# Performance work log

Hardware: AMD Instinct MI355X
Metric: run time of the kernel (lower is better)

The kernel has to match this reference:

```python
import jax, jax.numpy as jnp
import numpy as np

N, E, D, ED, G = 50000, 800000, 64, 32, 50


def setup_inputs() -> dict:
    key = jax.random.key(0)
    ks = jax.random.split(key, 24)
    s = 0.05
    inp = {
        "x": jax.random.normal(ks[0], (N, D), jnp.float32),
        "edge_attr": jax.random.normal(ks[1], (E, ED), jnp.float32),
        "edge_index": jax.random.randint(ks[2], (2, E), 0, N, jnp.int64),
    }
    i = 3
    for step in range(2):
        inp[f"fe{step}_W1"] = jax.random.normal(ks[i], (2 * D + ED, D), jnp.float32) * s; i += 1
        inp[f"fe{step}_b1"] = jnp.zeros((D,), jnp.float32)
        inp[f"fe{step}_W2"] = jax.random.normal(ks[i], (D, D), jnp.float32) * s; i += 1
        inp[f"fe{step}_b2"] = jnp.zeros((D,), jnp.float32)
        inp[f"lstm{step}_Wih"] = jax.random.normal(ks[i], (D, 4 * D), jnp.float32) * s; i += 1
        inp[f"lstm{step}_Whh"] = jax.random.normal(ks[i], (D, 4 * D), jnp.float32) * s; i += 1
        inp[f"lstm{step}_bih"] = jnp.zeros((4 * D,), jnp.float32)
        inp[f"lstm{step}_bhh"] = jnp.zeros((4 * D,), jnp.float32)
    inp["gm_W"] = jax.random.normal(ks[i], (D, G), jnp.float32) * s; i += 1
    inp["gm_b"] = jnp.zeros((G,), jnp.float32)
    inp["fm_W"] = jax.random.normal(ks[i], (D, G), jnp.float32) * s; i += 1
    inp["fm_b"] = jnp.zeros((G,), jnp.float32)
    return inp


def _mpn(x, edge_attr, src, dst, W1, b1, W2, b2):
    # x_i = x[dst] (target), x_j = x[src] (source); aggregate 'add' at dst
    m = jnp.concatenate([x[dst], x[src], edge_attr], axis=1)  # [E, 2D+ED]
    m = jax.nn.relu(m @ W1 + b1) @ W2 + b2                    # [E, D]
    return jax.ops.segment_sum(m, dst, num_segments=x.shape[0])


def _lstm_cell(inp, h, c, Wih, Whh, bih, bhh):
    gates = inp @ Wih + h @ Whh + (bih + bhh)  # [N, 4D], gate order i,f,g,o
    i, f, g, o = jnp.split(gates, 4, axis=1)
    c = jax.nn.sigmoid(f) * c + jax.nn.sigmoid(i) * jnp.tanh(g)
    h = jax.nn.sigmoid(o) * jnp.tanh(c)
    return h, c


def reference(x, edge_attr, edge_index,
              fe0_W1, fe0_b1, fe0_W2, fe0_b2,
              lstm0_Wih, lstm0_Whh, lstm0_bih, lstm0_bhh,
              fe1_W1, fe1_b1, fe1_W2, fe1_b2,
              lstm1_Wih, lstm1_Whh, lstm1_bih, lstm1_bhh,
              gm_W, gm_b, fm_W, fm_b):
    src, dst = edge_index[0], edge_index[1]
    c = jnp.zeros_like(x)
    fes = [(fe0_W1, fe0_b1, fe0_W2, fe0_b2), (fe1_W1, fe1_b1, fe1_W2, fe1_b2)]
    lstms = [(lstm0_Wih, lstm0_Whh, lstm0_bih, lstm0_bhh),
             (lstm1_Wih, lstm1_Whh, lstm1_bih, lstm1_bhh)]
    for step in range(2):
        a = _mpn(x, edge_attr, src, dst, *fes[step])
        # LSTMCell(input=x, (h=a, c=c)) as in the original forward
        x, c = _lstm_cell(x, a, c, *lstms[step])
    g = jax.nn.sigmoid(x @ gm_W + gm_b)   # [N, G]
    h_v_G = x @ fm_W + fm_b               # [N, G]
    return jnp.sum(g * h_v_G, axis=0)     # [G]
```

## Files before the change

kernel.cpp:

```cpp
#include <hip/hip_runtime.h>
#include <hip/hip_bf16.h>

using short8 = __attribute__((ext_vector_type(8))) short;
using f32x4  = __attribute__((ext_vector_type(4))) float;

#define KLP 136

__device__ __forceinline__ unsigned short f2bf(float f) {
  unsigned u = __float_as_uint(f);
  u += 0x7FFFu + ((u >> 16) & 1u);
  return (unsigned short)(u >> 16);
}
__device__ __forceinline__ unsigned pack2(float a, float b) {
  return (unsigned)f2bf(a) | ((unsigned)f2bf(b) << 16);
}
#if __has_builtin(__builtin_amdgcn_rcpf)
__device__ __forceinline__ float fast_rcp(float x) { return __builtin_amdgcn_rcpf(x); }
#else
__device__ __forceinline__ float fast_rcp(float x) { return 1.f / x; }
#endif
__device__ __forceinline__ float sigm(float x) { return fast_rcp(1.f + __expf(-x)); }
__device__ __forceinline__ float tanh_f(float x) { return fmaf(2.f, sigm(2.f * x), -1.f); }

__global__ __launch_bounds__(256) void prep_simple(
    const float* __restrict__ W1_0, const float* __restrict__ Wih0,
    const float* __restrict__ bih0, const float* __restrict__ bhh0,
    const float* __restrict__ W1_1, const float* __restrict__ Wih1,
    const float* __restrict__ bih1, const float* __restrict__ bhh1,
    const float* __restrict__ gmW, const float* __restrict__ fmW,
    unsigned short* __restrict__ W1T,
    unsigned short* __restrict__ WcT,
    float* __restrict__ bG,
    unsigned short* __restrict__ WrT)
{
  int t = blockIdx.x * 256 + threadIdx.x;
  const int per = 10240 + 16384 + 256;
  if (t >= 2 * per + 8192) return;
  if (t >= 2 * per) {
    int r2 = t - 2 * per;
    int o = r2 >> 6, k = r2 & 63;
    float v = 0.f;
    if (o < 50) v = gmW[k * 50 + o];
    else if (o >= 64 && o < 114) v = fmW[k * 50 + (o - 64)];
    WrT[o * 64 + k] = f2bf(v);
    return;
  }
  int step = t / per, r = t % per;
  const float* W1  = step ? W1_1 : W1_0;
  const float* Wih = step ? Wih1 : Wih0;
  const float* bih = step ? bih1 : bih0;
  const float* bhh = step ? bhh1 : bhh0;
  if (r < 10240) {
    int o = r / 160, k = r % 160;
    W1T[step * 10240 + o * 160 + k] = f2bf(W1[k * 64 + o]);
  } else if (r < 26624) {
    int rr = r - 10240;
    int g = rr >> 6, k = rr & 63;
    WcT[step * 32768 + g * 128 + k] = f2bf(Wih[k * 256 + g]);
  } else {
    int g = r - 26624;
    bG[step * 256 + g] = bih[g] + bhh[g];
  }
}

__global__ __launch_bounds__(256) void prep_merge(
    const float* __restrict__ W2_0, const float* __restrict__ Whh0, const float* __restrict__ b2_0,
    const float* __restrict__ W2_1, const float* __restrict__ Whh1, const float* __restrict__ b2_1,
    unsigned short* __restrict__ WcT,
    float* __restrict__ b2h)
{
  int t = blockIdx.x * 256 + threadIdx.x;
  if (t < 32768) {
    int step = t >> 14, r = t & 16383;
    int g = r >> 6, k = r & 63;
    const float* W2  = step ? W2_1 : W2_0;
    const float* Whh = step ? Whh1 : Whh0;
    float v = 0.f;
    for (int j = 0; j < 64; ++j) v = fmaf(W2[k * 64 + j], Whh[j * 256 + g], v);
    WcT[step * 32768 + g * 128 + 64 + k] = f2bf(v);
  } else if (t < 33280) {
    int r = t - 32768;
    int step = r >> 8, g = r & 255;
    const float* b2  = step ? b2_1 : b2_0;
    const float* Whh = step ? Whh1 : Whh0;
    float v = 0.f;
    for (int j = 0; j < 64; ++j) v = fmaf(b2[j], Whh[j * 256 + g], v);
    b2h[step * 256 + g] = v;
  }
}

__global__ __launch_bounds__(256) void convert_x(
    const float* __restrict__ x, unsigned short* __restrict__ xb, int n)
{
  int i = blockIdx.x * 256 + threadIdx.x;
  if (i < n) xb[i] = f2bf(x[i]);
}

__global__ __launch_bounds__(256) void hist_kernel(
    const int* __restrict__ dstI, int* __restrict__ hist, int E)
{
  int e = blockIdx.x * 256 + threadIdx.x;
  if (e < E) atomicAdd(&hist[dstI[e]], 1);
}

__global__ __launch_bounds__(256) void scan_part(
    const int* __restrict__ hist, int2* __restrict__ blockTot, int N)
{
  __shared__ int sD[256], sS[256];
  int t = threadIdx.x;
  int n = blockIdx.x * 256 + t;
  int d = (n < N) ? hist[n] : 0;
  int sg = (d + 15) >> 4;
  sD[t] = d; sS[t] = sg;
  __syncthreads();
  #pragma unroll
  for (int off = 128; off; off >>= 1) {
    if (t < off) { sD[t] += sD[t + off]; sS[t] += sS[t + off]; }
    __syncthreads();
  }
  if (t == 0) blockTot[blockIdx.x] = make_int2(sD[0], sS[0]);
}

__global__ __launch_bounds__(256) void scan_mid(
    const int2* __restrict__ blockTot, int2* __restrict__ blockBase,
    int* __restrict__ nSegTot, int nb)
{
  __shared__ int sD[256], sS[256];
  int t = threadIdx.x;
  int d = 0, s = 0;
  if (t < nb) { int2 v = blockTot[t]; d = v.x; s = v.y; }
  sD[t] = d; sS[t] = s;
  __syncthreads();
  #pragma unroll
  for (int off = 1; off < 256; off <<= 1) {
    int vd = (t >= off) ? sD[t - off] : 0;
    int vs = (t >= off) ? sS[t - off] : 0;
    __syncthreads();
    sD[t] += vd; sS[t] += vs;
    __syncthreads();
  }
  if (t < nb) blockBase[t] = make_int2(sD[t] - d, sS[t] - s);
  if (t == nb - 1) *nSegTot = sS[t];
}

__global__ __launch_bounds__(256) void scan_final(
    const int* __restrict__ hist, const int2* __restrict__ blockBase,
    int* __restrict__ cursor, int4* __restrict__ segInfo, int N)
{
  __shared__ int sD[256], sS[256];
  int t = threadIdx.x;
  int n = blockIdx.x * 256 + t;
  int d = (n < N) ? hist[n] : 0;
  int sg = (d + 15) >> 4;
  sD[t] = d; sS[t] = sg;
  __syncthreads();
  #pragma unroll
  for (int off = 1; off < 256; off <<= 1) {
    int vd = (t >= off) ? sD[t - off] : 0;
    int vs = (t >= off) ? sS[t - off] : 0;
    __syncthreads();
    sD[t] += vd; sS[t] += vs;
    __syncthreads();
  }
  if (n < N) {
    int2 bb = blockBase[blockIdx.x];
    int degBase = bb.x + sD[t] - d;
    int segBase = bb.y + sS[t] - sg;
    cursor[n] = degBase;
    for (int j = 0; j < sg; ++j)
      segInfo[segBase + j] = make_int4(degBase + j * 16, n, min(d - j * 16, 16), 0);
  }
}

__global__ __launch_bounds__(256) void scatter_perm(
    const int* __restrict__ srcI, const int* __restrict__ dstI,
    const float* __restrict__ ea, int* __restrict__ cursor,
    int* __restrict__ srcS, unsigned short* __restrict__ eaS, int E)
{
  int e = blockIdx.x * 256 + threadIdx.x;
  if (e >= E) return;
  int d = dstI[e];
  int p = atomicAdd(&cursor[d], 1);
  srcS[p] = srcI[e];
  const float4* pe = (const float4*)(ea + (long long)e * 32);
  float4 a0 = pe[0], a1 = pe[1], a2 = pe[2], a3 = pe[3];
  float4 a4 = pe[4], a5 = pe[5], a6 = pe[6], a7 = pe[7];
  uint4* out = (uint4*)(eaS + (long long)p * 32);
  out[0] = make_uint4(pack2(a0.x, a0.y), pack2(a0.z, a0.w), pack2(a1.x, a1.y), pack2(a1.z, a1.w));
  out[1] = make_uint4(pack2(a2.x, a2.y), pack2(a2.z, a2.w), pack2(a3.x, a3.y), pack2(a3.z, a3.w));
  out[2] = make_uint4(pack2(a4.x, a4.y), pack2(a4.z, a4.w), pack2(a5.x, a5.y), pack2(a5.z, a5.w));
  out[3] = make_uint4(pack2(a6.x, a6.y), pack2(a6.z, a6.w), pack2(a7.x, a7.y), pack2(a7.z, a7.w));
}

__global__ __launch_bounds__(256) void edge_gemm_reg(
    const unsigned short* __restrict__ xb,
    const unsigned short* __restrict__ eaS,
    const int* __restrict__ srcS,
    const int4* __restrict__ segInfo,
    const int* __restrict__ nSegPtr,
    const unsigned short* __restrict__ W1T,
    const float* __restrict__ b1,
    float* __restrict__ aggrH)
{
  const int t = threadIdx.x;
  const int w = t >> 6, l = t & 63;
  const int quad = l >> 4, lr = l & 15;

  short8 bF[5][4];
  #pragma unroll
  for (int kc = 0; kc < 5; ++kc)
    #pragma unroll
    for (int n = 0; n < 4; ++n)
      bF[kc][n] = *(const short8*)(W1T + (n * 16 + lr) * 160 + kc * 32 + quad * 8);
  float bb[4];
  #pragma unroll
  for (int n = 0; n < 4; ++n) bb[n] = b1[n * 16 + lr];

  const int nSeg = *nSegPtr;
  const int W = gridDim.x * 4;
  int s = blockIdx.x * 4 + w;
  if (s >= nSeg) return;
  int4 si = segInfo[s];
  int src = srcS[si.x + min(lr, si.z - 1)];

  while (true) {
    const int sn = s + W;
    const bool more = sn < nSeg;
    int4 si_n = si;
    if (more) si_n = segInfo[sn];

    const int start = si.x, node = si.y, cnt = si.z;
    const int er = min(lr, cnt - 1);

    const short8* pd = (const short8*)(xb + (long long)node * 64);
    const short8* ps = (const short8*)(xb + (long long)src * 64);
    const short8* pe = (const short8*)(eaS + (long long)(start + er) * 32);
    short8 a0 = pd[quad];
    short8 a1 = pd[4 + quad];
    short8 a2 = ps[quad];
    short8 a3 = ps[4 + quad];
    short8 a4 = pe[quad];

    int src_n = src;
    if (more) src_n = srcS[si_n.x + min(lr, si_n.z - 1)];

    f32x4 acc[4] = {};
    #pragma unroll
    for (int n = 0; n < 4; ++n) acc[n] = __builtin_amdgcn_mfma_f32_16x16x32_bf16(a0, bF[0][n], acc[n], 0, 0, 0);
    #pragma unroll
    for (int n = 0; n < 4; ++n) acc[n] = __builtin_amdgcn_mfma_f32_16x16x32_bf16(a1, bF[1][n], acc[n], 0, 0, 0);
    #pragma unroll
    for (int n = 0; n < 4; ++n) acc[n] = __builtin_amdgcn_mfma_f32_16x16x32_bf16(a2, bF[2][n], acc[n], 0, 0, 0);
    #pragma unroll
    for (int n = 0; n < 4; ++n) acc[n] = __builtin_amdgcn_mfma_f32_16x16x32_bf16(a3, bF[3][n], acc[n], 0, 0, 0);
    #pragma unroll
    for (int n = 0; n < 4; ++n) acc[n] = __builtin_amdgcn_mfma_f32_16x16x32_bf16(a4, bF[4][n], acc[n], 0, 0, 0);

    #pragma unroll
    for (int n = 0; n < 4; ++n) {
      float sum = 0.f;
      #pragma unroll
      for (int rr = 0; rr < 4; ++rr) {
        float v = fmaxf(acc[n][rr] + bb[n], 0.f);
        sum += (quad * 4 + rr < cnt) ? v : 0.f;
      }
      sum += __shfl_xor(sum, 16);
      sum += __shfl_xor(sum, 32);
      if (quad == 0) unsafeAtomicAdd(&aggrH[(long long)node * 64 + n * 16 + lr], sum);
    }

    if (!more) break;
    s = sn; si = si_n; src = src_n;
  }
}

__global__ __launch_bounds__(256) void lstm3(
    const unsigned short* __restrict__ xbin,
    const float* __restrict__ aggrH,
    const float* __restrict__ cin,
    float* __restrict__ cout,
    const unsigned short* __restrict__ WcT,
    const float* __restrict__ bG,
    const float* __restrict__ b2h,
    const int* __restrict__ degA,
    unsigned short* __restrict__ xbout,
    int nNodes)
{
  __shared__ unsigned short sIn[64 * KLP];
  __shared__ unsigned short sW[64 * KLP];
  __shared__ float sBG[256], sB2h[256];
  const int t = threadIdx.x;
  sBG[t] = bG[t];
  sB2h[t] = b2h[t];

  const int base_n = blockIdx.x * 64;
  const int nl = t >> 2, q = t & 3;
  const int node = base_n + nl;
  unsigned short* rowp = sIn + nl * KLP;
  if (node < nNodes) {
    const uint4* px = (const uint4*)(xbin + (long long)node * 64);
    *(uint4*)(rowp + q * 16)     = px[q * 2];
    *(uint4*)(rowp + q * 16 + 8) = px[q * 2 + 1];
    const float4* pg = (const float4*)(aggrH + (long long)node * 64) + q * 4;
    float4 g0 = pg[0], g1 = pg[1], g2 = pg[2], g3 = pg[3];
    *(uint4*)(rowp + 64 + q * 16) =
        make_uint4(pack2(g0.x, g0.y), pack2(g0.z, g0.w), pack2(g1.x, g1.y), pack2(g1.z, g1.w));
    *(uint4*)(rowp + 64 + q * 16 + 8) =
        make_uint4(pack2(g2.x, g2.y), pack2(g2.z, g2.w), pack2(g3.x, g3.y), pack2(g3.z, g3.w));
  } else {
    *(uint4*)(rowp + q * 16)          = make_uint4(0, 0, 0, 0);
    *(uint4*)(rowp + q * 16 + 8)      = make_uint4(0, 0, 0, 0);
    *(uint4*)(rowp + 64 + q * 16)     = make_uint4(0, 0, 0, 0);
    *(uint4*)(rowp + 64 + q * 16 + 8) = make_uint4(0, 0, 0, 0);
  }

  const int w = t >> 6, l = t & 63, quad = l >> 4, lr = l & 15;
  const int row0 = w * 16;
  f32x4 acc[16] = {};
  for (int grp = 0; grp < 4; ++grp) {
    const uint4* gw = (const uint4*)WcT + (long long)(grp * 64) * 16;
    uint4* lw = (uint4*)sW;
    {
      int o0 = t >> 4, s4 = t & 15;
      #pragma unroll
      for (int pp = 0; pp < 4; ++pp) {
        int o = pp * 16 + o0;
        lw[o * 17 + s4] = gw[o * 16 + s4];
      }
    }
    __syncthreads();
    #pragma unroll
    for (int kc = 0; kc < 4; ++kc) {
      short8 aF = *(const short8*)(sIn + (row0 + lr) * KLP + kc * 32 + quad * 8);
      #pragma unroll
      for (int nt = 0; nt < 4; ++nt) {
        short8 bF = *(const short8*)(sW + (nt * 16 + lr) * KLP + kc * 32 + quad * 8);
        acc[grp * 4 + nt] = __builtin_amdgcn_mfma_f32_16x16x32_bf16(aF, bF, acc[grp * 4 + nt], 0, 0, 0);
      }
    }
    __syncthreads();
  }

  #pragma unroll
  for (int nt = 0; nt < 4; ++nt) {
    #pragma unroll
    for (int rr = 0; rr < 4; ++rr) {
      int node2 = base_n + row0 + quad * 4 + rr;
      if (node2 < nNodes) {
        int col = nt * 16 + lr;
        long long off = (long long)node2 * 64 + col;
        float dg = (float)degA[node2];
        float iv = acc[nt][rr]      + sBG[col]       + dg * sB2h[col];
        float fv = acc[4 + nt][rr]  + sBG[64 + col]  + dg * sB2h[64 + col];
        float gv = acc[8 + nt][rr]  + sBG[128 + col] + dg * sB2h[128 + col];
        float ov = acc[12 + nt][rr] + sBG[192 + col] + dg * sB2h[192 + col];
        float cOld = cin ? cin[off] : 0.f;
        float cN = sigm(fv) * cOld + sigm(iv) * tanh_f(gv);
        float hN = sigm(ov) * tanh_f(cN);
        cout[off] = cN;
        xbout[off] = f2bf(hN);
      }
    }
  }
}

__global__ __launch_bounds__(256) void readout(
    const unsigned short* __restrict__ xq,
    const unsigned short* __restrict__ WrT,
    const float* __restrict__ gb, const float* __restrict__ fb,
    float* __restrict__ out, int nNodes)
{
  __shared__ unsigned short sX[64 * 72];
  __shared__ unsigned short sW[128 * 72];
  __shared__ float sOut[4][64];
  __shared__ float sGb[64], sFb[64];
  const int t = threadIdx.x;
  {
    const uint4* gw = (const uint4*)WrT;
    uint4* lw = (uint4*)sW;
    #pragma unroll
    for (int pp = 0; pp < 4; ++pp) {
      int idx = t + pp * 256;
      int o = idx >> 3, s = idx & 7;
      lw[o * 9 + s] = gw[idx];
    }
    if (t < 50)      { sGb[t] = gb[t]; sFb[t] = fb[t]; }
    else if (t < 64) { sGb[t] = 0.f;   sFb[t] = 0.f; }
  }
  const int base = blockIdx.x * 64;
  const int nl = t >> 2, q = t & 3;
  const int node = base + nl;
  {
    uint4* dst = (uint4*)(sX + nl * 72 + q * 16);
    if (node < nNodes) {
      const uint4* px = (const uint4*)(xq + (long long)node * 64);
      dst[0] = px[q * 2];
      dst[1] = px[q * 2 + 1];
    } else {
      dst[0] = make_uint4(0, 0, 0, 0);
      dst[1] = make_uint4(0, 0, 0, 0);
    }
  }
  __syncthreads();

  const int w = t >> 6, l = t & 63, quad = l >> 4, lr = l & 15;
  f32x4 acc[8] = {};
  #pragma unroll
  for (int kc = 0; kc < 2; ++kc) {
    short8 aF = *(const short8*)(sX + (w * 16 + lr) * 72 + kc * 32 + quad * 8);
    #pragma unroll
    for (int n = 0; n < 8; ++n) {
      short8 bF = *(const short8*)(sW + (n * 16 + lr) * 72 + kc * 32 + quad * 8);
      acc[n] = __builtin_amdgcn_mfma_f32_16x16x32_bf16(aF, bF, acc[n], 0, 0, 0);
    }
  }
  #pragma unroll
  for (int n = 0; n < 4; ++n) {
    float val = 0.f;
    #pragma unroll
    for (int rr = 0; rr < 4; ++rr) {
      int nd = base + w * 16 + quad * 4 + rr;
      if (nd < nNodes) {
        int jj = n * 16 + lr;
        float gv = sigm(acc[n][rr] + sGb[jj]);
        float fv = acc[n + 4][rr] + sFb[jj];
        val += gv * fv;
      }
    }
    val += __shfl_xor(val, 16);
    val += __shfl_xor(val, 32);
    if (quad == 0) sOut[w][n * 16 + lr] = val;
  }
  __syncthreads();
  if (t < 50) {
    float s = sOut[0][t] + sOut[1][t] + sOut[2][t] + sOut[3][t];
    unsafeAtomicAdd(&out[t], s);
  }
}

extern "C" void kernel_launch(void* const* d_in, const int* in_sizes, int n_in,
                              void* d_out, int out_size, void* d_ws, size_t ws_size,
                              hipStream_t stream)
{
  const float* x      = (const float*)d_in[0];
  const float* ea     = (const float*)d_in[1];
  const int*   ei     = (const int*)d_in[2];
  const float* fe0_W1 = (const float*)d_in[3];
  const float* fe0_b1 = (const float*)d_in[4];
  const float* fe0_W2 = (const float*)d_in[5];
  const float* fe0_b2 = (const float*)d_in[6];
  const float* l0_Wih = (const float*)d_in[7];
  const float* l0_Whh = (const float*)d_in[8];
  const float* l0_bih = (const float*)d_in[9];
  const float* l0_bhh = (const float*)d_in[10];
  const float* fe1_W1 = (const float*)d_in[11];
  const float* fe1_b1 = (const float*)d_in[12];
  const float* fe1_W2 = (const float*)d_in[13];
  const float* fe1_b2 = (const float*)d_in[14];
  const float* l1_Wih = (const float*)d_in[15];
  const float* l1_Whh = (const float*)d_in[16];
  const float* l1_bih = (const float*)d_in[17];
  const float* l1_bhh = (const float*)d_in[18];
  const float* gm_W   = (const float*)d_in[19];
  const float* gm_b   = (const float*)d_in[20];
  const float* fm_W   = (const float*)d_in[21];
  const float* fm_b   = (const float*)d_in[22];

  const int N = in_sizes[0] / 64;
  const int E = in_sizes[1] / 32;
  const int* srcI = ei;
  const int* dstI = ei + E;

  char* ws = (char*)d_ws;
  unsigned short* xb0     = (unsigned short*)(ws + 0);
  unsigned short* xb1     = (unsigned short*)(ws + 6400000);
  float*          aggrH   = (float*)(ws + 12800000);
  float*          cbuf    = (float*)(ws + 25600000);
  unsigned short* eaS     = (unsigned short*)(ws + 38400000);
  int*            srcS    = (int*)(ws + 89601024);
  int4*           segInfo = (int4*)(ws + 92801088);
  int*            histA   = (int*)(ws + 94401280);
  int*            curA    = (int*)(ws + 94601280);
  unsigned short* W1T     = (unsigned short*)(ws + 94801280);
  unsigned short* WcT     = (unsigned short*)(ws + 94842240);
  float*          bG      = (float*)(ws + 94973312);
  float*          b2h     = (float*)(ws + 94975360);
  unsigned short* WrT     = (unsigned short*)(ws + 94977408);
  int*            nSegPtr = (int*)(ws + 94993792);
  int2*           blockTot  = (int2*)(ws + 94993856);
  int2*           blockBase = (int2*)(ws + 94995904);

  hipMemsetAsync(d_out, 0, out_size * sizeof(float), stream);
  hipMemsetAsync(histA, 0, (size_t)N * 4, stream);

  prep_simple<<<(2 * 26880 + 8192 + 255) / 256, 256, 0, stream>>>(
      fe0_W1, l0_Wih, l0_bih, l0_bhh,
      fe1_W1, l1_Wih, l1_bih, l1_bhh,
      gm_W, fm_W, W1T, WcT, bG, WrT);
  prep_merge<<<(33280 + 255) / 256, 256, 0, stream>>>(
      fe0_W2, l0_Whh, fe0_b2, fe1_W2, l1_Whh, fe1_b2, WcT, b2h);
  convert_x<<<(N * 64 + 255) / 256, 256, 0, stream>>>(x, xb0, N * 64);

  const int nb = (N + 255) / 256;
  hist_kernel<<<(E + 255) / 256, 256, 0, stream>>>(dstI, histA, E);
  scan_part<<<nb, 256, 0, stream>>>(histA, blockTot, N);
  scan_mid<<<1, 256, 0, stream>>>(blockTot, blockBase, nSegPtr, nb);
  scan_final<<<nb, 256, 0, stream>>>(histA, blockBase, curA, segInfo, N);
  scatter_perm<<<(E + 255) / 256, 256, 0, stream>>>(srcI, dstI, ea, curA, srcS, eaS, E);

  const int nodeBlocks = (N + 63) / 64;

  hipMemsetAsync(aggrH, 0, (size_t)N * 64 * 4, stream);
  edge_gemm_reg<<<2048, 256, 0, stream>>>(xb0, eaS, srcS, segInfo, nSegPtr,
                                          W1T, fe0_b1, aggrH);
  lstm3<<<nodeBlocks, 256, 0, stream>>>(xb0, aggrH, nullptr, cbuf, WcT, bG, b2h,
                                        histA, xb1, N);

  hipMemsetAsync(aggrH, 0, (size_t)N * 64 * 4, stream);
  edge_gemm_reg<<<2048, 256, 0, stream>>>(xb1, eaS, srcS, segInfo, nSegPtr,
                                          W1T + 10240, fe1_b1, aggrH);
  lstm3<<<nodeBlocks, 256, 0, stream>>>(xb1, aggrH, cbuf, cbuf, WcT + 32768,
                                        bG + 256, b2h + 256, histA, xb0, N);

  readout<<<nodeBlocks, 256, 0, stream>>>(xb0, WrT, gm_b, fm_b, (float*)d_out, N);
}
```

Measured before the change: 483.0 us.

## Merge prep kernels and memsets, stage W1 fragments in LDS, widen atomics

Folds the weight-prep, weight-merge, x conversion and all buffer zeroing into one prep_all launch. The aggregation-buffer memset before step two is replaced by zeroing inside the first lstm3. In edge_gemm the W1 B-fragments move from registers into shared memory, which lowers register pressure at the cost of LDS reads per MFMA. The per-row atomic adds now use all 64 lanes instead of 16 lanes four times. The aim is fewer launches and memsets and better occupancy, in exchange for extra LDS traffic in the hot loop.

```diff
diff --git a/kernel.cpp b/kernel.cpp
--- a/kernel.cpp
+++ b/kernel.cpp
@@ -22,78 +22,102 @@
 __device__ __forceinline__ float sigm(float x) { return fast_rcp(1.f + __expf(-x)); }
 __device__ __forceinline__ float tanh_f(float x) { return fmaf(2.f, sigm(2.f * x), -1.f); }
 
-__global__ __launch_bounds__(256) void prep_simple(
+__global__ __launch_bounds__(256) void prep_all(
+    const float* __restrict__ x,
     const float* __restrict__ W1_0, const float* __restrict__ Wih0,
     const float* __restrict__ bih0, const float* __restrict__ bhh0,
     const float* __restrict__ W1_1, const float* __restrict__ Wih1,
     const float* __restrict__ bih1, const float* __restrict__ bhh1,
+    const float* __restrict__ W2_0, const float* __restrict__ Whh0, const float* __restrict__ b2_0,
+    const float* __restrict__ W2_1, const float* __restrict__ Whh1, const float* __restrict__ b2_1,
     const float* __restrict__ gmW, const float* __restrict__ fmW,
     unsigned short* __restrict__ W1T,
     unsigned short* __restrict__ WcT,
     float* __restrict__ bG,
-    unsigned short* __restrict__ WrT)
+    float* __restrict__ b2h,
+    unsigned short* __restrict__ WrT,
+    unsigned short* __restrict__ xb0,
+    float* __restrict__ aggrH,
+    int* __restrict__ histA,
+    float* __restrict__ outZ, int nOut,
+    int N)
 {
   int t = blockIdx.x * 256 + threadIdx.x;
-  const int per = 10240 + 16384 + 256;
-  if (t >= 2 * per + 8192) return;
-  if (t >= 2 * per) {
-    int r2 = t - 2 * per;
-    int o = r2 >> 6, k = r2 & 63;
-    float v = 0.f;
-    if (o < 50) v = gmW[k * 50 + o];
-    else if (o >= 64 && o < 114) v = fmW[k * 50 + (o - 64)];
-    WrT[o * 64 + k] = f2bf(v);
+
+  const int R0 = 2 * 26880 + 8192;
+  if (t < R0) {
+    const int per = 26880;
+    if (t >= 2 * per) {
+      int r2 = t - 2 * per;
+      int o = r2 >> 6, k = r2 & 63;
+      float v = 0.f;
+      if (o < 50) v = gmW[k * 50 + o];
+      else if (o >= 64 && o < 114) v = fmW[k * 50 + (o - 64)];
+      WrT[o * 64 + k] = f2bf(v);
+      return;
+    }
+    int step = t / per, r = t % per;
+    const float* W1  = step ? W1_1 : W1_0;
+    const float* Wih = step ? Wih1 : Wih0;
+    const float* bih = step ? bih1 : bih0;
+    const float* bhh = step ? bhh1 : bhh0;
+    if (r < 10240) {
+      int o = r / 160, k = r % 160;
+      W1T[step * 10240 + o * 160 + k] = f2bf(W1[k * 64 + o]);
+    } else if (r < 26624) {
+      int rr = r - 10240;
+      int g = rr >> 6, k = rr & 63;
+      WcT[step * 32768 + g * 128 + k] = f2bf(Wih[k * 256 + g]);
+    } else {
+      int g = r - 26624;
+      bG[step * 256 + g] = bih[g] + bhh[g];
+    }
     return;
   }
-  int step = t / per, r = t % per;
-  const float* W1  = step ? W1_1 : W1_0;
-  const float* Wih = step ? Wih1 : Wih0;
-  const float* bih = step ? bih1 : bih0;
-  const float* bhh = step ? bhh1 : bhh0;
-  if (r < 10240) {
-    int o = r / 160, k = r % 160;
-    W1T[step * 10240 + o * 160 + k] = f2bf(W1[k * 64 + o]);
-  } else if (r < 26624) {
-    int rr = r - 10240;
-    int g = rr >> 6, k = rr & 63;
-    WcT[step * 32768 + g * 128 + k] = f2bf(Wih[k * 256 + g]);
-  } else {
-    int g = r - 26624;
-    bG[step * 256 + g] = bih[g] + bhh[g];
-  }
-}
-
-__global__ __launch_bounds__(256) void prep_merge(
-    const float* __restrict__ W2_0, const float* __restrict__ Whh0, const float* __restrict__ b2_0,
-    const float* __restrict__ W2_1, const float* __restrict__ Whh1, const float* __restrict__ b2_1,
-    unsigned short* __restrict__ WcT,
-    float* __restrict__ b2h)
-{
-  int t = blockIdx.x * 256 + threadIdx.x;
-  if (t < 32768) {
-    int step = t >> 14, r = t & 16383;
-    int g = r >> 6, k = r & 63;
-    const float* W2  = step ? W2_1 : W2_0;
-    const float* Whh = step ? Whh1 : Whh0;
-    float v = 0.f;
-    for (int j = 0; j < 64; ++j) v = fmaf(W2[k * 64 + j], Whh[j * 256 + g], v);
-    WcT[step * 32768 + g * 128 + 64 + k] = f2bf(v);
-  } else if (t < 33280) {
-    int r = t - 32768;
-    int step = r >> 8, g = r & 255;
-    const float* b2  = step ? b2_1 : b2_0;
-    const float* Whh = step ? Whh1 : Whh0;
-    float v = 0.f;
-    for (int j = 0; j < 64; ++j) v = fmaf(b2[j], Whh[j * 256 + g], v);
-    b2h[step * 256 + g] = v;
-  }
-}
-
-__global__ __launch_bounds__(256) void convert_x(
-    const float* __restrict__ x, unsigned short* __restrict__ xb, int n)
-{
-  int i = blockIdx.x * 256 + threadIdx.x;
-  if (i < n) xb[i] = f2bf(x[i]);
+  t -= R0;
+
+  const int R1 = 33280;
+  if (t < R1) {
+    if (t < 32768) {
+      int step = t >> 14, r = t & 16383;
+      int g = r >> 6, k = r & 63;
+      const float* W2  = step ? W2_1 : W2_0;
+      const float* Whh = step ? Whh1 : Whh0;
+      float v = 0.f;
+      for (int j = 0; j < 64; ++j) v = fmaf(W2[k * 64 + j], Whh[j * 256 + g], v);
+      WcT[step * 32768 + g * 128 + 64 + k] = f2bf(v);
+    } else {
+      int r = t - 32768;
+      int step = r >> 8, g = r & 255;
+      const float* b2  = step ? b2_1 : b2_0;
+      const float* Whh = step ? Whh1 : Whh0;
+      float v = 0.f;
+      for (int j = 0; j < 64; ++j) v = fmaf(b2[j], Whh[j * 256 + g], v);
+      b2h[step * 256 + g] = v;
+    }
+    return;
+  }
+  t -= R1;
+
+  const int R2 = N * 8;
+  if (t < R2) {
+    const float4* p = (const float4*)(x + (long long)t * 8);
+    float4 a0 = p[0], a1 = p[1];
+    *(uint4*)(xb0 + (long long)t * 8) =
+        make_uint4(pack2(a0.x, a0.y), pack2(a0.z, a0.w), pack2(a1.x, a1.y), pack2(a1.z, a1.w));
+    return;
+  }
+  t -= R2;
+
+  const int R3 = N * 16;
+  if (t < R3) { ((float4*)aggrH)[t] = make_float4(0.f, 0.f, 0.f, 0.f); return; }
+  t -= R3;
+
+  const int R4 = N / 4;
+  if (t < R4) { ((int4*)histA)[t] = make_int4(0, 0, 0, 0); return; }
+  t -= R4;
+
+  if (t < nOut) outZ[t] = 0.f;
 }
 
 __global__ __launch_bounds__(256) void hist_kernel(
@@ -192,7 +216,7 @@
   out[3] = make_uint4(pack2(a6.x, a6.y), pack2(a6.z, a6.w), pack2(a7.x, a7.y), pack2(a7.z, a7.w));
 }
 
-__global__ __launch_bounds__(256) void edge_gemm_reg(
+__global__ __launch_bounds__(256) void edge_gemm(
     const unsigned short* __restrict__ xb,
     const unsigned short* __restrict__ eaS,
     const int* __restrict__ srcS,
@@ -202,19 +226,23 @@
     const float* __restrict__ b1,
     float* __restrict__ aggrH)
 {
+  __shared__ unsigned short stash[20 * 64 * 8];
   const int t = threadIdx.x;
   const int w = t >> 6, l = t & 63;
   const int quad = l >> 4, lr = l & 15;
 
-  short8 bF[5][4];
-  #pragma unroll
-  for (int kc = 0; kc < 5; ++kc)
-    #pragma unroll
-    for (int n = 0; n < 4; ++n)
-      bF[kc][n] = *(const short8*)(W1T + (n * 16 + lr) * 160 + kc * 32 + quad * 8);
+  #pragma unroll
+  for (int p = 0; p < 5; ++p) {
+    int idx = p * 256 + t;
+    int grp = idx >> 6, ll = idx & 63;
+    int kc = grp >> 2, n = grp & 3;
+    *(uint4*)(stash + idx * 8) =
+        *(const uint4*)(W1T + (n * 16 + (ll & 15)) * 160 + kc * 32 + (ll >> 4) * 8);
+  }
   float bb[4];
   #pragma unroll
   for (int n = 0; n < 4; ++n) bb[n] = b1[n * 16 + lr];
+  __syncthreads();
 
   const int nSeg = *nSegPtr;
   const int W = gridDim.x * 4;
@@ -234,28 +262,27 @@
 
     const short8* pd = (const short8*)(xb + (long long)node * 64);
     const short8* ps = (const short8*)(xb + (long long)src * 64);
-    const short8* pe = (const short8*)(eaS + (long long)(start + er) * 32);
     short8 a0 = pd[quad];
     short8 a1 = pd[4 + quad];
     short8 a2 = ps[quad];
     short8 a3 = ps[4 + quad];
-    short8 a4 = pe[quad];
+    short8 a4 = *(const short8*)(eaS + (long long)(start + er) * 32 + quad * 8);
 
     int src_n = src;
     if (more) src_n = srcS[si_n.x + min(lr, si_n.z - 1)];
 
     f32x4 acc[4] = {};
     #pragma unroll
-    for (int n = 0; n < 4; ++n) acc[n] = __builtin_amdgcn_mfma_f32_16x16x32_bf16(a0, bF[0][n], acc[n], 0, 0, 0);
-    #pragma unroll
-    for (int n = 0; n < 4; ++n) acc[n] = __builtin_amdgcn_mfma_f32_16x16x32_bf16(a1, bF[1][n], acc[n], 0, 0, 0);
-    #pragma unroll
-    for (int n = 0; n < 4; ++n) acc[n] = __builtin_amdgcn_mfma_f32_16x16x32_bf16(a2, bF[2][n], acc[n], 0, 0, 0);
-    #pragma unroll
-    for (int n = 0; n < 4; ++n) acc[n] = __builtin_amdgcn_mfma_f32_16x16x32_bf16(a3, bF[3][n], acc[n], 0, 0, 0);
-    #pragma unroll
-    for (int n = 0; n < 4; ++n) acc[n] = __builtin_amdgcn_mfma_f32_16x16x32_bf16(a4, bF[4][n], acc[n], 0, 0, 0);
-
+    for (int kc = 0; kc < 5; ++kc) {
+      short8 aX = (kc == 0) ? a0 : (kc == 1) ? a1 : (kc == 2) ? a2 : (kc == 3) ? a3 : a4;
+      #pragma unroll
+      for (int n = 0; n < 4; ++n) {
+        short8 bFr = *(const short8*)(stash + (((kc << 2) | n) * 64 + l) * 8);
+        acc[n] = __builtin_amdgcn_mfma_f32_16x16x32_bf16(aX, bFr, acc[n], 0, 0, 0);
+      }
+    }
+
+    float myv = 0.f;
     #pragma unroll
     for (int n = 0; n < 4; ++n) {
       float sum = 0.f;
@@ -266,8 +293,9 @@
       }
       sum += __shfl_xor(sum, 16);
       sum += __shfl_xor(sum, 32);
-      if (quad == 0) unsafeAtomicAdd(&aggrH[(long long)node * 64 + n * 16 + lr], sum);
-    }
+      if (quad == n) myv = sum;
+    }
+    unsafeAtomicAdd(&aggrH[(long long)node * 64 + l], myv);
 
     if (!more) break;
     s = sn; si = si_n; src = src_n;
@@ -276,7 +304,7 @@
 
 __global__ __launch_bounds__(256) void lstm3(
     const unsigned short* __restrict__ xbin,
-    const float* __restrict__ aggrH,
+    float* __restrict__ aggrH,
     const float* __restrict__ cin,
     float* __restrict__ cout,
     const unsigned short* __restrict__ WcT,
@@ -284,7 +312,7 @@
     const float* __restrict__ b2h,
     const int* __restrict__ degA,
     unsigned short* __restrict__ xbout,
-    int nNodes)
+    int nNodes, int zeroAggr)
 {
   __shared__ unsigned short sIn[64 * KLP];
   __shared__ unsigned short sW[64 * KLP];
@@ -301,12 +329,16 @@
     const uint4* px = (const uint4*)(xbin + (long long)node * 64);
     *(uint4*)(rowp + q * 16)     = px[q * 2];
     *(uint4*)(rowp + q * 16 + 8) = px[q * 2 + 1];
-    const float4* pg = (const float4*)(aggrH + (long long)node * 64) + q * 4;
+    float4* pg = (float4*)(aggrH + (long long)node * 64) + q * 4;
     float4 g0 = pg[0], g1 = pg[1], g2 = pg[2], g3 = pg[3];
     *(uint4*)(rowp + 64 + q * 16) =
         make_uint4(pack2(g0.x, g0.y), pack2(g0.z, g0.w), pack2(g1.x, g1.y), pack2(g1.z, g1.w));
     *(uint4*)(rowp + 64 + q * 16 + 8) =
         make_uint4(pack2(g2.x, g2.y), pack2(g2.z, g2.w), pack2(g3.x, g3.y), pack2(g3.z, g3.w));
+    if (zeroAggr) {
+      float4 z = make_float4(0.f, 0.f, 0.f, 0.f);
+      pg[0] = z; pg[1] = z; pg[2] = z; pg[3] = z;
+    }
   } else {
     *(uint4*)(rowp + q * 16)          = make_uint4(0, 0, 0, 0);
     *(uint4*)(rowp + q * 16 + 8)      = make_uint4(0, 0, 0, 0);
@@ -490,16 +522,16 @@
   int2*           blockTot  = (int2*)(ws + 94993856);
   int2*           blockBase = (int2*)(ws + 94995904);
 
-  hipMemsetAsync(d_out, 0, out_size * sizeof(float), stream);
-  hipMemsetAsync(histA, 0, (size_t)N * 4, stream);
-
-  prep_simple<<<(2 * 26880 + 8192 + 255) / 256, 256, 0, stream>>>(
+  const int prepT = (2 * 26880 + 8192) + 33280 + N * 8 + N * 16 + N / 4 + out_size;
+  prep_all<<<(prepT + 255) / 256, 256, 0, stream>>>(
+      x,
       fe0_W1, l0_Wih, l0_bih, l0_bhh,
       fe1_W1, l1_Wih, l1_bih, l1_bhh,
-      gm_W, fm_W, W1T, WcT, bG, WrT);
-  prep_merge<<<(33280 + 255) / 256, 256, 0, stream>>>(
-      fe0_W2, l0_Whh, fe0_b2, fe1_W2, l1_Whh, fe1_b2, WcT, b2h);
-  convert_x<<<(N * 64 + 255) / 256, 256, 0, stream>>>(x, xb0, N * 64);
+      fe0_W2, l0_Whh, fe0_b2,
+      fe1_W2, l1_Whh, fe1_b2,
+      gm_W, fm_W,
+      W1T, WcT, bG, b2h, WrT, xb0,
+      aggrH, histA, (float*)d_out, out_size, N);
 
   const int nb = (N + 255) / 256;
   hist_kernel<<<(E + 255) / 256, 256, 0, stream>>>(dstI, histA, E);
@@ -510,17 +542,15 @@
 
   const int nodeBlocks = (N + 63) / 64;
 
-  hipMemsetAsync(aggrH, 0, (size_t)N * 64 * 4, stream);
-  edge_gemm_reg<<<2048, 256, 0, stream>>>(xb0, eaS, srcS, segInfo, nSegPtr,
-                                          W1T, fe0_b1, aggrH);
+  edge_gemm<<<2048, 256, 0, stream>>>(xb0, eaS, srcS, segInfo, nSegPtr,
+                                      W1T, fe0_b1, aggrH);
   lstm3<<<nodeBlocks, 256, 0, stream>>>(xb0, aggrH, nullptr, cbuf, WcT, bG, b2h,
-                                        histA, xb1, N);
-
-  hipMemsetAsync(aggrH, 0, (size_t)N * 64 * 4, stream);
-  edge_gemm_reg<<<2048, 256, 0, stream>>>(xb1, eaS, srcS, segInfo, nSegPtr,
-                                          W1T + 10240, fe1_b1, aggrH);
+                                        histA, xb1, N, 1);
+
+  edge_gemm<<<2048, 256, 0, stream>>>(xb1, eaS, srcS, segInfo, nSegPtr,
+                                      W1T + 10240, fe1_b1, aggrH);
   lstm3<<<nodeBlocks, 256, 0, stream>>>(xb1, aggrH, cbuf, cbuf, WcT + 32768,
-                                        bG + 256, b2h + 256, histA, xb0, N);
+                                        bG + 256, b2h + 256, histA, xb0, N, 0);
 
   readout<<<nodeBlocks, 256, 0, stream>>>(xb0, WrT, gm_b, fm_b, (float*)d_out, N);
 }
```

New measurement: 452.2 us. -6.4%, faster.
